# Optimization experiments

Hardware: AMD Instinct MI355X
Metric: run time of the kernel (lower is better)

The kernel has to match this reference:

```python
import jax, jax.numpy as jnp
import numpy as np

N_NODES = 100000
N_EDGES = 625000
D_IN = 128
D_OUT = 128
N_ETYPES = 64


def setup_inputs() -> dict:
    key = jax.random.key(0)
    k1, k2, k3, k4, k5, k6 = jax.random.split(key, 6)
    node_features = jax.random.normal(k1, (N_NODES, D_IN), dtype=jnp.float32)
    edge_index = jax.random.randint(k2, (2, N_EDGES), 0, N_NODES, dtype=jnp.int64)
    edge_type = jax.random.randint(k3, (N_EDGES,), 0, N_ETYPES, dtype=jnp.int64)
    edge_emb = jax.random.normal(k4, (N_ETYPES, D_OUT), dtype=jnp.float32)
    W = jax.random.normal(k5, (D_IN, D_OUT), dtype=jnp.float32) / np.sqrt(D_IN)
    b = jax.random.normal(k6, (D_OUT,), dtype=jnp.float32) * 0.01
    return {"node_features": node_features, "edge_index": edge_index,
            "edge_type": edge_type, "edge_emb": edge_emb, "W": W, "b": b}


def reference(node_features, edge_index, edge_type, edge_emb, W, b):
    # Linear transform of node features: (N, D_out)
    h = node_features @ W + b
    src, tgt = edge_index[0], edge_index[1]
    # Per-edge message: gather src feature + edge-type embedding  (E, D_out)
    messages = h[src] + edge_emb[edge_type]
    # Scatter-add into target nodes
    aggregated = jax.ops.segment_sum(messages, tgt, num_segments=N_NODES)
    # Self contribution + ReLU
    return jax.nn.relu(aggregated + h)
```

## Files before the change

### kernel.cpp

```cpp
#include <hip/hip_runtime.h>
#include <hip/hip_bf16.h>

#define D 128

typedef __attribute__((ext_vector_type(8))) short short8v;
typedef __attribute__((ext_vector_type(4))) float float4v;

__device__ __forceinline__ unsigned short f2bf(float f) {
  union { float f; unsigned int u; } v; v.f = f;
  unsigned int r = v.u + 0x7fffu + ((v.u >> 16) & 1u);
  return (unsigned short)(r >> 16);
}
__device__ __forceinline__ unsigned int pkbf(float lo, float hi) {
  float2 f; f.x = lo; f.y = hi;
  __hip_bfloat162 v = __float22bfloat162_rn(f);
  union { __hip_bfloat162 b; unsigned int u; } c; c.b = v;
  return c.u;
}
__device__ __forceinline__ float bflo(unsigned int u) {
  union { unsigned int v; float f; } c; c.v = u << 16; return c.f;
}
__device__ __forceinline__ float bfhi(unsigned int u) {
  union { unsigned int v; float f; } c; c.v = u & 0xffff0000u; return c.f;
}

__global__ __launch_bounds__(256) void prep_kernel(
    const float* __restrict__ W, const float* __restrict__ eemb,
    unsigned short* __restrict__ Wt, unsigned short* __restrict__ em_bf,
    unsigned short* __restrict__ h_bf, int n_nodes) {
  int i = blockIdx.x * 256 + threadIdx.x;
  if (i < D * D) Wt[i] = f2bf(W[(i & 127) * D + (i >> 7)]);
  if (i < 64 * D) em_bf[i] = f2bf(eemb[i]);
  if (i < 64) ((unsigned int*)(h_bf + (size_t)n_nodes * D))[i] = 0u;
  if (i >= 64 && i < 128) ((unsigned int*)(em_bf + 64 * D))[i - 64] = 0u;
}

#define XS_STRIDE 138
__global__ __launch_bounds__(256) void gemm_h_kernel(
    const float* __restrict__ nf, const unsigned short* __restrict__ Wt,
    const float* __restrict__ b, unsigned short* __restrict__ h_bf,
    int n_nodes) {
  __shared__ unsigned short Xs[64 * XS_STRIDE];
  const int tid = threadIdx.x;
  const int nodeBase = blockIdx.x * 64;

  #pragma unroll
  for (int s = 0; s < 4; ++s) {
    const int row = (tid >> 4) + s * 16;
    const int col = (tid & 15) * 8;
    uint4 sv = {0u, 0u, 0u, 0u};
    if (nodeBase + row < n_nodes) {
      const float4* p = (const float4*)&nf[(size_t)(nodeBase + row) * D + col];
      float4 a = p[0], c = p[1];
      sv.x = pkbf(a.x, a.y);
      sv.y = pkbf(a.z, a.w);
      sv.z = pkbf(c.x, c.y);
      sv.w = pkbf(c.z, c.w);
    }
    *(uint4*)&Xs[row * XS_STRIDE + col] = sv;
  }

  const int w = tid >> 6;
  const int l = tid & 63;
  const int m = l & 15;
  const int q = l >> 4;
  const int n0 = (w & 1) * 64;
  const int nodeHalf = (w >> 1) * 32;

  short8v afrag[4][4];
  #pragma unroll
  for (int nt = 0; nt < 4; ++nt) {
    const int n = n0 + nt * 16 + m;
    #pragma unroll
    for (int kc = 0; kc < 4; ++kc)
      afrag[nt][kc] = *(const short8v*)&Wt[n * D + kc * 32 + q * 8];
  }

  float4v acc[4][2] = {};
  __syncthreads();

  #pragma unroll
  for (int kc = 0; kc < 4; ++kc) {
    #pragma unroll
    for (int t = 0; t < 2; ++t) {
      const int node = nodeHalf + t * 16 + m;
      const short8v bv =
          *(const short8v*)&Xs[node * XS_STRIDE + kc * 32 + q * 8];
      #pragma unroll
      for (int nt = 0; nt < 4; ++nt)
        acc[nt][t] = __builtin_amdgcn_mfma_f32_16x16x32_bf16(
            afrag[nt][kc], bv, acc[nt][t], 0, 0, 0);
    }
  }

  #pragma unroll
  for (int nt = 0; nt < 4; ++nt) {
    const int colBase = n0 + nt * 16 + q * 4;
    const float4 bv = *(const float4*)&b[colBase];
    #pragma unroll
    for (int t = 0; t < 2; ++t) {
      const int node = nodeBase + nodeHalf + t * 16 + m;
      if (node < n_nodes) {
        uint2 val;
        val.x = pkbf(acc[nt][t][0] + bv.x, acc[nt][t][1] + bv.y);
        val.y = pkbf(acc[nt][t][2] + bv.z, acc[nt][t][3] + bv.w);
        *(uint2*)&h_bf[(size_t)node * D + colBase] = val;
      }
    }
  }
}

__global__ __launch_bounds__(256) void hist_kernel(
    const int* __restrict__ eidx, int* __restrict__ counts, int n_edges) {
  int e = blockIdx.x * 256 + threadIdx.x;
  if (e < n_edges) atomicAdd(&counts[eidx[n_edges + e]], 1);
}

__global__ __launch_bounds__(256) void scan1_kernel(
    const int* __restrict__ counts, int* __restrict__ offsets,
    int* __restrict__ blockSums, int n) {
  __shared__ int lds[256];
  const int tid = threadIdx.x;
  const int base = blockIdx.x * 1024 + tid * 4;
  int v[4];
  #pragma unroll
  for (int k = 0; k < 4; ++k) v[k] = (base + k < n) ? counts[base + k] : 0;
  int s = v[0] + v[1] + v[2] + v[3];
  lds[tid] = s;
  for (int off = 1; off < 256; off <<= 1) {
    __syncthreads();
    int t = (tid >= off) ? lds[tid - off] : 0;
    __syncthreads();
    lds[tid] += t;
  }
  __syncthreads();
  int run = lds[tid] - s;
  #pragma unroll
  for (int k = 0; k < 4; ++k) {
    if (base + k < n) offsets[base + k] = run;
    run += v[k];
  }
  if (tid == 255) blockSums[blockIdx.x] = lds[255];
}

__global__ __launch_bounds__(1024) void scan2_kernel(int* __restrict__ blockSums,
                                                     int* __restrict__ blockOffs,
                                                     int nb) {
  __shared__ int lds[1024];
  const int tid = threadIdx.x;
  int v = (tid < nb) ? blockSums[tid] : 0;
  lds[tid] = v;
  for (int off = 1; off < 1024; off <<= 1) {
    __syncthreads();
    int t = (tid >= off) ? lds[tid - off] : 0;
    __syncthreads();
    lds[tid] += t;
  }
  __syncthreads();
  if (tid < nb) blockOffs[tid] = lds[tid] - v;
}

__global__ __launch_bounds__(256) void scan3_kernel(
    int* __restrict__ offsets, int* __restrict__ cursor,
    const int* __restrict__ blockOffs, int n, int n_edges) {
  const int tid = threadIdx.x;
  const int add = blockOffs[blockIdx.x];
  const int base = blockIdx.x * 1024 + tid * 4;
  #pragma unroll
  for (int k = 0; k < 4; ++k) {
    int i = base + k;
    if (i < n) {
      int o = offsets[i] + add;
      offsets[i] = o;
      cursor[i] = o;
    }
  }
  if (blockIdx.x == 0 && tid == 0) offsets[n] = n_edges;
}

__global__ __launch_bounds__(256) void scatter_kernel(
    const int* __restrict__ eidx, const int* __restrict__ etype,
    int* __restrict__ cursor, unsigned int* __restrict__ packed, int n_edges) {
  int e = blockIdx.x * 256 + threadIdx.x;
  if (e >= n_edges) return;
  const int src = eidx[e];
  const int tgt = eidx[n_edges + e];
  const int et = etype[e];
  const int pos = atomicAdd(&cursor[tgt], 1);
  packed[pos] = (unsigned int)src | ((unsigned int)et << 17);
}

__global__ __launch_bounds__(256) void aggregate_kernel(
    const int* __restrict__ offsets, const unsigned int* __restrict__ packed,
    const uint2* __restrict__ e4, const uint2* __restrict__ h4,
    float* __restrict__ out, int n_nodes, int n_edges, unsigned int zero_p) {
  const int gid = blockIdx.x * 256 + threadIdx.x;
  const int lane = threadIdx.x & 63;
  const int half = lane >> 5;
  const int sl = lane & 31;
  const int n = (gid >> 6) * 2 + half;
  if (n >= n_nodes) return;

  const uint2 sb = h4[(size_t)n * 32 + sl];
  float a0 = bflo(sb.x), a1 = bfhi(sb.x), a2 = bflo(sb.y), a3 = bfhi(sb.y);
  float c0 = 0.f, c1 = 0.f, c2 = 0.f, c3 = 0.f;

  int j = offsets[n];
  const int end = offsets[n + 1];
  int trips = (end - j + 3) >> 2;
  int to = __shfl_xor(trips, 32);
  const int T = trips > to ? trips : to;
  const int emax = n_edges - 1;

  for (int t = 0; t < T; ++t, j += 4) {
    const int j1 = j + 1, j2 = j + 2, j3 = j + 3;
    unsigned int p0 = packed[j  <= emax ? j  : emax];
    unsigned int p1 = packed[j1 <= emax ? j1 : emax];
    unsigned int p2 = packed[j2 <= emax ? j2 : emax];
    unsigned int p3 = packed[j3 <= emax ? j3 : emax];
    p0 = (j  < end) ? p0 : zero_p;
    p1 = (j1 < end) ? p1 : zero_p;
    p2 = (j2 < end) ? p2 : zero_p;
    p3 = (j3 < end) ? p3 : zero_p;
    const uint2 g0 = h4[(size_t)(p0 & 0x1FFFFu) * 32 + sl];
    const uint2 g1 = h4[(size_t)(p1 & 0x1FFFFu) * 32 + sl];
    const uint2 g2 = h4[(size_t)(p2 & 0x1FFFFu) * 32 + sl];
    const uint2 g3 = h4[(size_t)(p3 & 0x1FFFFu) * 32 + sl];
    const uint2 e0 = e4[(p0 >> 17) * 32 + sl];
    const uint2 e1 = e4[(p1 >> 17) * 32 + sl];
    const uint2 e2 = e4[(p2 >> 17) * 32 + sl];
    const uint2 e3 = e4[(p3 >> 17) * 32 + sl];
    a0 += bflo(g0.x) + bflo(e0.x); a1 += bfhi(g0.x) + bfhi(e0.x);
    a2 += bflo(g0.y) + bflo(e0.y); a3 += bfhi(g0.y) + bfhi(e0.y);
    c0 += bflo(g1.x) + bflo(e1.x); c1 += bfhi(g1.x) + bfhi(e1.x);
    c2 += bflo(g1.y) + bflo(e1.y); c3 += bfhi(g1.y) + bfhi(e1.y);
    a0 += bflo(g2.x) + bflo(e2.x); a1 += bfhi(g2.x) + bfhi(e2.x);
    a2 += bflo(g2.y) + bflo(e2.y); a3 += bfhi(g2.y) + bfhi(e2.y);
    c0 += bflo(g3.x) + bflo(e3.x); c1 += bfhi(g3.x) + bfhi(e3.x);
    c2 += bflo(g3.y) + bflo(e3.y); c3 += bfhi(g3.y) + bfhi(e3.y);
  }

  float4 r;
  r.x = fmaxf(a0 + c0, 0.f);
  r.y = fmaxf(a1 + c1, 0.f);
  r.z = fmaxf(a2 + c2, 0.f);
  r.w = fmaxf(a3 + c3, 0.f);
  ((float4*)out)[(size_t)n * 32 + sl] = r;
}

extern "C" void kernel_launch(void* const* d_in, const int* in_sizes, int n_in,
                              void* d_out, int out_size, void* d_ws,
                              size_t ws_size, hipStream_t stream) {
  const float* nf   = (const float*)d_in[0];
  const int*   eidx = (const int*)d_in[1];
  const int*   etyp = (const int*)d_in[2];
  const float* eemb = (const float*)d_in[3];
  const float* W    = (const float*)d_in[4];
  const float* b    = (const float*)d_in[5];

  const int n_nodes = in_sizes[0] / D;
  const int n_edges = in_sizes[2];

  float* out = (float*)d_out;

  char* base = (char*)d_ws;
  unsigned short* Wt = (unsigned short*)base;
  unsigned short* em_bf = (unsigned short*)(base + 32768);
  unsigned short* h_bf = (unsigned short*)(base + 65536);
  char* tail = base + 65536 + (size_t)(n_nodes + 1) * D * 2;
  int* counts = (int*)tail;
  int* offsets = counts + n_nodes;
  int* cursor = offsets + (n_nodes + 1);
  int* blockSums = cursor + n_nodes;
  int* blockOffs = blockSums + 1024;
  unsigned int* packed = (unsigned int*)(blockOffs + 1024);

  const int nb = (n_nodes + 1023) / 1024;

  prep_kernel<<<64, 256, 0, stream>>>(W, eemb, Wt, em_bf, h_bf, n_nodes);

  gemm_h_kernel<<<(n_nodes + 63) / 64, 256, 0, stream>>>(nf, Wt, b, h_bf,
                                                         n_nodes);

  (void)hipMemsetAsync(counts, 0, (size_t)n_nodes * 4, stream);
  hist_kernel<<<(n_edges + 255) / 256, 256, 0, stream>>>(eidx, counts, n_edges);
  scan1_kernel<<<nb, 256, 0, stream>>>(counts, offsets, blockSums, n_nodes);
  scan2_kernel<<<1, 1024, 0, stream>>>(blockSums, blockOffs, nb);
  scan3_kernel<<<nb, 256, 0, stream>>>(offsets, cursor, blockOffs, n_nodes,
                                       n_edges);
  scatter_kernel<<<(n_edges + 255) / 256, 256, 0, stream>>>(eidx, etyp, cursor,
                                                            packed, n_edges);

  const unsigned int zero_p = (unsigned int)n_nodes | (64u << 17);
  const int aggBlocks = (n_nodes + 7) / 8;
  aggregate_kernel<<<aggBlocks, 256, 0, stream>>>(
      offsets, packed, (const uint2*)em_bf, (const uint2*)h_bf, out, n_nodes,
      n_edges, zero_p);
}
```

Measured before the change: 148.1 us.

## Fuse histogram into GEMM, merge scan passes, vectorize scatter, unroll gather by 8

New measurement: 143.3 us. 1.03x faster.

```diff
diff --git a/kernel.cpp b/kernel.cpp
--- a/kernel.cpp
+++ b/kernel.cpp
@@ -27,19 +27,22 @@
 __global__ __launch_bounds__(256) void prep_kernel(
     const float* __restrict__ W, const float* __restrict__ eemb,
     unsigned short* __restrict__ Wt, unsigned short* __restrict__ em_bf,
-    unsigned short* __restrict__ h_bf, int n_nodes) {
+    unsigned short* __restrict__ h_bf, int* __restrict__ counts,
+    int n_nodes) {
   int i = blockIdx.x * 256 + threadIdx.x;
   if (i < D * D) Wt[i] = f2bf(W[(i & 127) * D + (i >> 7)]);
   if (i < 64 * D) em_bf[i] = f2bf(eemb[i]);
   if (i < 64) ((unsigned int*)(h_bf + (size_t)n_nodes * D))[i] = 0u;
   if (i >= 64 && i < 128) ((unsigned int*)(em_bf + 64 * D))[i - 64] = 0u;
+  if (i < n_nodes) counts[i] = 0;
 }
 
 #define XS_STRIDE 138
 __global__ __launch_bounds__(256) void gemm_h_kernel(
     const float* __restrict__ nf, const unsigned short* __restrict__ Wt,
     const float* __restrict__ b, unsigned short* __restrict__ h_bf,
-    int n_nodes) {
+    const int* __restrict__ eidx_tgt, int* __restrict__ counts,
+    int n_nodes, int n_edges, int epb) {
   __shared__ unsigned short Xs[64 * XS_STRIDE];
   const int tid = threadIdx.x;
   const int nodeBase = blockIdx.x * 64;
@@ -108,12 +111,12 @@
       }
     }
   }
-}
-
-__global__ __launch_bounds__(256) void hist_kernel(
-    const int* __restrict__ eidx, int* __restrict__ counts, int n_edges) {
-  int e = blockIdx.x * 256 + threadIdx.x;
-  if (e < n_edges) atomicAdd(&counts[eidx[n_edges + e]], 1);
+
+  const int ebase = blockIdx.x * epb;
+  int eend = ebase + epb;
+  if (eend > n_edges) eend = n_edges;
+  for (int e = ebase + tid; e < eend; e += 256)
+    atomicAdd(&counts[eidx_tgt[e]], 1);
 }
 
 __global__ __launch_bounds__(256) void scan1_kernel(
@@ -143,29 +146,21 @@
   if (tid == 255) blockSums[blockIdx.x] = lds[255];
 }
 
-__global__ __launch_bounds__(1024) void scan2_kernel(int* __restrict__ blockSums,
-                                                     int* __restrict__ blockOffs,
-                                                     int nb) {
-  __shared__ int lds[1024];
+__global__ __launch_bounds__(256) void scan23_kernel(
+    int* __restrict__ offsets, int* __restrict__ cursor,
+    const int* __restrict__ blockSums, int nb, int n, int n_edges) {
+  __shared__ int lds[256];
   const int tid = threadIdx.x;
-  int v = (tid < nb) ? blockSums[tid] : 0;
-  lds[tid] = v;
-  for (int off = 1; off < 1024; off <<= 1) {
+  const int bid = blockIdx.x;
+  lds[tid] = (tid < bid && tid < nb) ? blockSums[tid] : 0;
+  __syncthreads();
+  #pragma unroll
+  for (int off = 128; off > 0; off >>= 1) {
+    if (tid < off) lds[tid] += lds[tid + off];
     __syncthreads();
-    int t = (tid >= off) ? lds[tid - off] : 0;
-    __syncthreads();
-    lds[tid] += t;
-  }
-  __syncthreads();
-  if (tid < nb) blockOffs[tid] = lds[tid] - v;
-}
-
-__global__ __launch_bounds__(256) void scan3_kernel(
-    int* __restrict__ offsets, int* __restrict__ cursor,
-    const int* __restrict__ blockOffs, int n, int n_edges) {
-  const int tid = threadIdx.x;
-  const int add = blockOffs[blockIdx.x];
-  const int base = blockIdx.x * 1024 + tid * 4;
+  }
+  const int add = lds[0];
+  const int base = bid * 1024 + tid * 4;
   #pragma unroll
   for (int k = 0; k < 4; ++k) {
     int i = base + k;
@@ -175,19 +170,32 @@
       cursor[i] = o;
     }
   }
-  if (blockIdx.x == 0 && tid == 0) offsets[n] = n_edges;
+  if (bid == 0 && tid == 0) offsets[n] = n_edges;
 }
 
 __global__ __launch_bounds__(256) void scatter_kernel(
     const int* __restrict__ eidx, const int* __restrict__ etype,
     int* __restrict__ cursor, unsigned int* __restrict__ packed, int n_edges) {
-  int e = blockIdx.x * 256 + threadIdx.x;
-  if (e >= n_edges) return;
-  const int src = eidx[e];
-  const int tgt = eidx[n_edges + e];
-  const int et = etype[e];
-  const int pos = atomicAdd(&cursor[tgt], 1);
-  packed[pos] = (unsigned int)src | ((unsigned int)et << 17);
+  const int e0 = (blockIdx.x * 256 + threadIdx.x) * 4;
+  if (e0 + 3 < n_edges) {
+    const int4 s4 = *(const int4*)&eidx[e0];
+    const int4 t4 = *(const int4*)&eidx[n_edges + e0];
+    const int4 y4 = *(const int4*)&etype[e0];
+    int pos;
+    pos = atomicAdd(&cursor[t4.x], 1);
+    packed[pos] = (unsigned int)s4.x | ((unsigned int)y4.x << 17);
+    pos = atomicAdd(&cursor[t4.y], 1);
+    packed[pos] = (unsigned int)s4.y | ((unsigned int)y4.y << 17);
+    pos = atomicAdd(&cursor[t4.z], 1);
+    packed[pos] = (unsigned int)s4.z | ((unsigned int)y4.z << 17);
+    pos = atomicAdd(&cursor[t4.w], 1);
+    packed[pos] = (unsigned int)s4.w | ((unsigned int)y4.w << 17);
+  } else {
+    for (int e = e0; e < n_edges; ++e) {
+      const int pos = atomicAdd(&cursor[eidx[n_edges + e]], 1);
+      packed[pos] = (unsigned int)eidx[e] | ((unsigned int)etype[e] << 17);
+    }
+  }
 }
 
 __global__ __launch_bounds__(256) void aggregate_kernel(
@@ -207,37 +215,37 @@
 
   int j = offsets[n];
   const int end = offsets[n + 1];
-  int trips = (end - j + 3) >> 2;
+  int trips = (end - j + 7) >> 3;
   int to = __shfl_xor(trips, 32);
   const int T = trips > to ? trips : to;
   const int emax = n_edges - 1;
 
-  for (int t = 0; t < T; ++t, j += 4) {
-    const int j1 = j + 1, j2 = j + 2, j3 = j + 3;
-    unsigned int p0 = packed[j  <= emax ? j  : emax];
-    unsigned int p1 = packed[j1 <= emax ? j1 : emax];
-    unsigned int p2 = packed[j2 <= emax ? j2 : emax];
-    unsigned int p3 = packed[j3 <= emax ? j3 : emax];
-    p0 = (j  < end) ? p0 : zero_p;
-    p1 = (j1 < end) ? p1 : zero_p;
-    p2 = (j2 < end) ? p2 : zero_p;
-    p3 = (j3 < end) ? p3 : zero_p;
-    const uint2 g0 = h4[(size_t)(p0 & 0x1FFFFu) * 32 + sl];
-    const uint2 g1 = h4[(size_t)(p1 & 0x1FFFFu) * 32 + sl];
-    const uint2 g2 = h4[(size_t)(p2 & 0x1FFFFu) * 32 + sl];
-    const uint2 g3 = h4[(size_t)(p3 & 0x1FFFFu) * 32 + sl];
-    const uint2 e0 = e4[(p0 >> 17) * 32 + sl];
-    const uint2 e1 = e4[(p1 >> 17) * 32 + sl];
-    const uint2 e2 = e4[(p2 >> 17) * 32 + sl];
-    const uint2 e3 = e4[(p3 >> 17) * 32 + sl];
-    a0 += bflo(g0.x) + bflo(e0.x); a1 += bfhi(g0.x) + bfhi(e0.x);
-    a2 += bflo(g0.y) + bflo(e0.y); a3 += bfhi(g0.y) + bfhi(e0.y);
-    c0 += bflo(g1.x) + bflo(e1.x); c1 += bfhi(g1.x) + bfhi(e1.x);
-    c2 += bflo(g1.y) + bflo(e1.y); c3 += bfhi(g1.y) + bfhi(e1.y);
-    a0 += bflo(g2.x) + bflo(e2.x); a1 += bfhi(g2.x) + bfhi(e2.x);
-    a2 += bflo(g2.y) + bflo(e2.y); a3 += bfhi(g2.y) + bfhi(e2.y);
-    c0 += bflo(g3.x) + bflo(e3.x); c1 += bfhi(g3.x) + bfhi(e3.x);
-    c2 += bflo(g3.y) + bflo(e3.y); c3 += bfhi(g3.y) + bfhi(e3.y);
+  for (int t = 0; t < T; ++t, j += 8) {
+    unsigned int p[8];
+    #pragma unroll
+    for (int u = 0; u < 8; ++u) {
+      const int ju = j + u;
+      const unsigned int pu = packed[ju <= emax ? ju : emax];
+      p[u] = (ju < end) ? pu : zero_p;
+    }
+    uint2 g[8], ev[8];
+    #pragma unroll
+    for (int u = 0; u < 8; ++u)
+      g[u] = h4[(size_t)(p[u] & 0x1FFFFu) * 32 + sl];
+    #pragma unroll
+    for (int u = 0; u < 8; ++u)
+      ev[u] = e4[(p[u] >> 17) * 32 + sl];
+    #pragma unroll
+    for (int u = 0; u < 8; u += 2) {
+      a0 += bflo(g[u].x) + bflo(ev[u].x);
+      a1 += bfhi(g[u].x) + bfhi(ev[u].x);
+      a2 += bflo(g[u].y) + bflo(ev[u].y);
+      a3 += bfhi(g[u].y) + bfhi(ev[u].y);
+      c0 += bflo(g[u + 1].x) + bflo(ev[u + 1].x);
+      c1 += bfhi(g[u + 1].x) + bfhi(ev[u + 1].x);
+      c2 += bflo(g[u + 1].y) + bflo(ev[u + 1].y);
+      c3 += bfhi(g[u + 1].y) + bfhi(ev[u + 1].y);
+    }
   }
 
   float4 r;
@@ -272,24 +280,24 @@
   int* offsets = counts + n_nodes;
   int* cursor = offsets + (n_nodes + 1);
   int* blockSums = cursor + n_nodes;
-  int* blockOffs = blockSums + 1024;
-  unsigned int* packed = (unsigned int*)(blockOffs + 1024);
+  unsigned int* packed = (unsigned int*)(blockSums + 1024);
 
   const int nb = (n_nodes + 1023) / 1024;
-
-  prep_kernel<<<64, 256, 0, stream>>>(W, eemb, Wt, em_bf, h_bf, n_nodes);
-
-  gemm_h_kernel<<<(n_nodes + 63) / 64, 256, 0, stream>>>(nf, Wt, b, h_bf,
-                                                         n_nodes);
-
-  (void)hipMemsetAsync(counts, 0, (size_t)n_nodes * 4, stream);
-  hist_kernel<<<(n_edges + 255) / 256, 256, 0, stream>>>(eidx, counts, n_edges);
+  const int gemmBlocks = (n_nodes + 63) / 64;
+  const int epb = (n_edges + gemmBlocks - 1) / gemmBlocks;
+
+  prep_kernel<<<(n_nodes + 255) / 256, 256, 0, stream>>>(W, eemb, Wt, em_bf,
+                                                         h_bf, counts, n_nodes);
+
+  gemm_h_kernel<<<gemmBlocks, 256, 0, stream>>>(
+      nf, Wt, b, h_bf, eidx + n_edges, counts, n_nodes, n_edges, epb);
+
   scan1_kernel<<<nb, 256, 0, stream>>>(counts, offsets, blockSums, n_nodes);
-  scan2_kernel<<<1, 1024, 0, stream>>>(blockSums, blockOffs, nb);
-  scan3_kernel<<<nb, 256, 0, stream>>>(offsets, cursor, blockOffs, n_nodes,
-                                       n_edges);
-  scatter_kernel<<<(n_edges + 255) / 256, 256, 0, stream>>>(eidx, etyp, cursor,
-                                                            packed, n_edges);
+  scan23_kernel<<<nb, 256, 0, stream>>>(offsets, cursor, blockSums, nb,
+                                        n_nodes, n_edges);
+
+  scatter_kernel<<<(n_edges + 1023) / 1024, 256, 0, stream>>>(
+      eidx, etyp, cursor, packed, n_edges);
 
   const unsigned int zero_p = (unsigned int)n_nodes | (64u << 17);
   const int aggBlocks = (n_nodes + 7) / 8;
```
